# Kernel optimization log

Hardware: AMD Instinct MI355X
Metric: run time of the kernel (lower is better)

## Reference

```python
import jax, jax.numpy as jnp
import numpy as np
from jax import lax

BETA = 0.5        # Sinkhron beta
N_ITER = 20       # got_iteration
THRESH = 0.1      # P > 0.1 threshold
NL_I = 5          # apply_non_linearity(..., 'elu', i=5)
EPS = 1e-9


def setup_inputs() -> dict:
    key = jax.random.key(0)
    k1, k2 = jax.random.split(key)
    B, N, D = 128, 512, 128
    h = jax.random.normal(k1, (B, N, D), dtype=jnp.float32)
    W0 = jnp.ones((D,), dtype=jnp.float32)
    W1 = jnp.ones((D,), dtype=jnp.float32)
    lengths = jax.random.randint(k2, (B,), 0, N, dtype=jnp.int32)
    return {"h": h, "W0": W0, "W1": W1, "lengths": lengths}


def _forward(h, W0, W1, lengths):
    B, N, D = h.shape
    lengths = jnp.maximum(lengths, 1)
    mask = (jnp.arange(N)[None, :] < lengths[:, None])          # [B, N] bool
    mf = mask.astype(h.dtype)
    mask2 = mf[:, :, None] * mf[:, None, :]                      # [B, N, N]

    # internal_forward: Diag layers with relu between (mlp_act='relu')
    h = h * W0
    h = jax.nn.relu(h)
    h = h * W1

    # cost_matrix_batch_torch: cosine similarity, add identity diag, mask
    hn = h / (jnp.linalg.norm(h, axis=-1, keepdims=True) + 1e-12)
    sim = jnp.einsum('bnd,bmd->bnm', hn, hn)                     # [B, N, N]
    sim = sim + jnp.eye(N, dtype=h.dtype)                        # add_eye_diag
    sim = sim * mask2
    cost = (1.0 - sim) * mask2

    # Sinkhorn with uniform marginals on valid nodes, fixed iterations
    n = lengths.astype(h.dtype)
    mu = mf / n[:, None]                                         # [B, N]
    K = jnp.exp(-cost / BETA) * mask2                            # [B, N, N]

    def body(carry, _):
        u, v = carry
        u = mu / (jnp.einsum('bnm,bm->bn', K, v) + EPS) * mf
        v = mu / (jnp.einsum('bnm,bn->bm', K, u) + EPS) * mf
        return (u, v), None

    (u, v), _ = lax.scan(body, (mf, mf), None, length=N_ITER)
    P = u[:, :, None] * K * v[:, None, :]                        # transport plan

    # P.detach(); scale by number of nodes per graph; threshold
    P = lax.stop_gradient(P)
    P = n[:, None, None] * P
    A = (P > THRESH).astype(h.dtype)
    similarity = A * sim
    # apply_non_linearity 'elu': elu(x*i - i) + 1
    out = jax.nn.elu(similarity * NL_I - NL_I) + 1.0
    return out


def reference(h, W0, W1, lengths):
    return _forward(h, W0, W1, lengths)
```

## Files before the change

kernel.cpp:

```cpp
#include <hip/hip_runtime.h>

#define BB 128
#define NN 512
#define DD 128
#define SLOT_STRIDE 544

__global__ __launch_bounds__(256) void hn_kernel(const float* __restrict__ h,
                                                 const float* __restrict__ W0,
                                                 const float* __restrict__ W1,
                                                 float* __restrict__ hn) {
    int wave = (int)((blockIdx.x * blockDim.x + threadIdx.x) >> 6);
    int lane = threadIdx.x & 63;
    const float2* h2 = (const float2*)(h + (size_t)wave * DD);
    float2 w0 = ((const float2*)W0)[lane];
    float2 w1 = ((const float2*)W1)[lane];
    float2 x = h2[lane];
    float p0 = fmaxf(x.x * w0.x, 0.0f) * w1.x;
    float p1 = fmaxf(x.y * w0.y, 0.0f) * w1.y;
    float ss = p0 * p0 + p1 * p1;
#pragma unroll
    for (int m = 32; m; m >>= 1) ss += __shfl_xor(ss, m);
    float inv = 1.0f / (sqrtf(ss) + 1e-12f);
    float2 o;
    o.x = p0 * inv;
    o.y = p1 * inv;
    ((float2*)(hn + (size_t)wave * DD))[lane] = o;
}

#define KC 32
__global__ __launch_bounds__(256) void sim_kernel(const float* __restrict__ hn,
                                                  const int* __restrict__ lengths,
                                                  float* __restrict__ K) {
    __shared__ float As[KC][132];
    __shared__ float Bs[KC][132];
    __shared__ int pre[BB + 1];
    int tid = threadIdx.x;
    if (tid == 0) {
        int acc = 0;
        for (int b = 0; b < BB; b++) {
            pre[b] = acc;
            int len = max(lengths[b], 1);
            int nt = (len + 127) >> 7;
            acc += nt * nt;
        }
        pre[BB] = acc;
    }
    __syncthreads();
    int total = pre[BB];

    int lr = tid >> 3;
    int lk = (tid & 7) << 2;
    int tx = tid & 15, ty = tid >> 4;

    for (int t = blockIdx.x; t < total; t += gridDim.x) {
        int lo = 0, hi = BB;
        while (lo + 1 < hi) {
            int mid = (lo + hi) >> 1;
            if (pre[mid] <= t) lo = mid; else hi = mid;
        }
        int b = lo;
        int local = t - pre[b];
        int len = max(lengths[b], 1);
        int nt = (len + 127) >> 7;
        int ti = local / nt;
        int tj = local - ti * nt;
        int r0 = ti << 7, c0 = tj << 7;
        const float* base = hn + (size_t)b * NN * DD;
        float acc[8][8] = {};

        for (int kc = 0; kc < DD; kc += KC) {
#pragma unroll
            for (int rr = 0; rr < 128; rr += 32) {
                float4 a = *(const float4*)(base + (size_t)(r0 + lr + rr) * DD + kc + lk);
                As[lk + 0][lr + rr] = a.x; As[lk + 1][lr + rr] = a.y;
                As[lk + 2][lr + rr] = a.z; As[lk + 3][lr + rr] = a.w;
                float4 bb = *(const float4*)(base + (size_t)(c0 + lr + rr) * DD + kc + lk);
                Bs[lk + 0][lr + rr] = bb.x; Bs[lk + 1][lr + rr] = bb.y;
                Bs[lk + 2][lr + rr] = bb.z; Bs[lk + 3][lr + rr] = bb.w;
            }
            __syncthreads();
#pragma unroll
            for (int kk = 0; kk < KC; kk++) {
                float4 a0 = *(const float4*)&As[kk][ty * 8];
                float4 a1 = *(const float4*)&As[kk][ty * 8 + 4];
                float4 b0 = *(const float4*)&Bs[kk][tx * 4];
                float4 b1 = *(const float4*)&Bs[kk][64 + tx * 4];
                float ar[8] = {a0.x, a0.y, a0.z, a0.w, a1.x, a1.y, a1.z, a1.w};
                float bc[8] = {b0.x, b0.y, b0.z, b0.w, b1.x, b1.y, b1.z, b1.w};
#pragma unroll
                for (int r = 0; r < 8; r++)
#pragma unroll
                    for (int c = 0; c < 8; c++)
                        acc[r][c] = fmaf(ar[r], bc[c], acc[r][c]);
            }
            __syncthreads();
        }
        float* out = K + (size_t)b * NN * NN;
#pragma unroll
        for (int r = 0; r < 8; r++) {
            int i = r0 + ty * 8 + r;
            if (i >= len) continue;
#pragma unroll
            for (int cg = 0; cg < 2; cg++) {
                int j0 = c0 + cg * 64 + tx * 4;
                if (j0 >= len) continue;
                float vv[4];
#pragma unroll
                for (int c = 0; c < 4; c++) {
                    float s = acc[r][cg * 4 + c] + ((i == j0 + c) ? 1.0f : 0.0f);
                    vv[c] = expf(2.0f * s - 2.0f);
                }
                float4 o;
                o.x = vv[0]; o.y = vv[1]; o.z = vv[2]; o.w = vv[3];
                *(float4*)(out + (size_t)i * NN + j0) = o;
            }
        }
    }
}

__device__ __forceinline__ float dot8(float4 A, float4 B, float4 x0, float4 x1) {
    float d = fmaf(A.x, x0.x, fmaf(A.y, x0.y, fmaf(A.z, x0.z, A.w * x0.w)));
    return fmaf(B.x, x1.x, fmaf(B.y, x1.y, fmaf(B.z, x1.z, fmaf(B.w, x1.w, d))));
}

__global__ __launch_bounds__(512, 4) void coop_sink(const float* __restrict__ K,
                                                    float* __restrict__ u_buf,
                                                    float* __restrict__ v_buf,
                                                    const int* __restrict__ lengths,
                                                    float* __restrict__ slots) {
    __shared__ float xb[NN];
    __shared__ float pv[8 * NN];
    __shared__ int Sh[16], Pre[16];

    int g = blockIdx.x;
    int x = g & 7;
    int j = g >> 3;
    int tid = threadIdx.x;

    if (tid == 0) {
        int need[16]; int ssum = 0;
        for (int m = 0; m < 16; m++) {
            int L = max(lengths[x + 8 * m], 1);
            need[m] = (L + 63) >> 6;
            ssum += need[m];
        }
        while (ssum > 64) {
            int best = 0, bv = need[0];
            for (int m = 1; m < 16; m++)
                if (need[m] > bv) { bv = need[m]; best = m; }
            need[best]--; ssum--;
        }
        int acc = 0;
        for (int m = 0; m < 16; m++) { Pre[m] = acc; Sh[m] = need[m]; acc += need[m]; }
    }
    __syncthreads();

    int m = -1;
    for (int mm = 0; mm < 16; mm++)
        if (j >= Pre[mm] && j < Pre[mm] + Sh[mm]) { m = mm; break; }
    if (m < 0) return;
    int b = x + 8 * m;
    int q = j - Pre[m];
    int S = Sh[m];
    int jbase = Pre[m];

    int len = max(lengths[b], 1);
    int len4 = (len + 3) & ~3;
    int rpq = (len + S - 1) / S;
    int r_lo = q * rpq;
    int nrows = min(len - r_lo, rpq);
    if (nrows < 0) nrows = 0;
    float inv_n = 1.0f / (float)len;

    int w = tid >> 6, l = tid & 63;
    int c0 = 4 * l, c1 = 256 + 4 * l;
    bool a0 = c0 < len4, a1 = c1 < len4;
    const float* Kb = K + (size_t)b * NN * NN;

    xb[tid] = (tid < len) ? 1.0f : 0.0f;

    float4 kA0 = {0,0,0,0}, kA1 = {0,0,0,0}, kA2 = {0,0,0,0}, kA3 = {0,0,0,0};
    float4 kA4 = {0,0,0,0}, kA5 = {0,0,0,0}, kA6 = {0,0,0,0}, kA7 = {0,0,0,0};
    float4 kB0 = {0,0,0,0}, kB1 = {0,0,0,0}, kB2 = {0,0,0,0}, kB3 = {0,0,0,0};
    float4 kB4 = {0,0,0,0}, kB5 = {0,0,0,0}, kB6 = {0,0,0,0}, kB7 = {0,0,0,0};
#define FILL_ROW(o)                                                          \
    {                                                                        \
        int i_ = w + 8 * o;                                                  \
        if (i_ < nrows) {                                                    \
            const float* g0_ = Kb + (size_t)(r_lo + i_) * NN;                \
            if (a0) kA##o = *(const float4*)(g0_ + c0);                      \
            if (a1) kB##o = *(const float4*)(g0_ + c1);                      \
        }                                                                    \
    }
    FILL_ROW(0) FILL_ROW(1) FILL_ROW(2) FILL_ROW(3)
    FILL_ROW(4) FILL_ROW(5) FILL_ROW(6) FILL_ROW(7)
#undef FILL_ROW

    __syncthreads();

    for (int t = 0; t < 20; t++) {
        float4 xv0 = *(const float4*)(xb + c0);
        float4 xv1 = *(const float4*)(xb + c1);
        float4 pa = {0, 0, 0, 0}, pb = {0, 0, 0, 0};

        float d0 = dot8(kA0, kB0, xv0, xv1);
        float d1 = dot8(kA1, kB1, xv0, xv1);
        float d2 = dot8(kA2, kB2, xv0, xv1);
        float d3 = dot8(kA3, kB3, xv0, xv1);
        float d4 = dot8(kA4, kB4, xv0, xv1);
        float d5 = dot8(kA5, kB5, xv0, xv1);
        float d6 = dot8(kA6, kB6, xv0, xv1);
        float d7 = dot8(kA7, kB7, xv0, xv1);
#pragma unroll
        for (int mm = 32; mm; mm >>= 1) {
            d0 += __shfl_xor(d0, mm); d1 += __shfl_xor(d1, mm);
            d2 += __shfl_xor(d2, mm); d3 += __shfl_xor(d3, mm);
            d4 += __shfl_xor(d4, mm); d5 += __shfl_xor(d5, mm);
            d6 += __shfl_xor(d6, mm); d7 += __shfl_xor(d7, mm);
        }
        float u0 = inv_n / (d0 + 1e-9f), u1 = inv_n / (d1 + 1e-9f);
        float u2 = inv_n / (d2 + 1e-9f), u3 = inv_n / (d3 + 1e-9f);
        float u4 = inv_n / (d4 + 1e-9f), u5 = inv_n / (d5 + 1e-9f);
        float u6 = inv_n / (d6 + 1e-9f), u7 = inv_n / (d7 + 1e-9f);
#define ACC_ROW(o, uo)                                                       \
    pa.x = fmaf(kA##o.x, uo, pa.x); pa.y = fmaf(kA##o.y, uo, pa.y);          \
    pa.z = fmaf(kA##o.z, uo, pa.z); pa.w = fmaf(kA##o.w, uo, pa.w);          \
    pb.x = fmaf(kB##o.x, uo, pb.x); pb.y = fmaf(kB##o.y, uo, pb.y);          \
    pb.z = fmaf(kB##o.z, uo, pb.z); pb.w = fmaf(kB##o.w, uo, pb.w);
        ACC_ROW(0, u0) ACC_ROW(1, u1) ACC_ROW(2, u2) ACC_ROW(3, u3)
        ACC_ROW(4, u4) ACC_ROW(5, u5) ACC_ROW(6, u6) ACC_ROW(7, u7)
#undef ACC_ROW
        if (t == 19 && l == 0) {
            float* ub = u_buf + (size_t)b * NN + r_lo + w;
            if (w + 0 < nrows) ub[0] = u0;
            if (w + 8 < nrows) ub[8] = u1;
            if (w + 16 < nrows) ub[16] = u2;
            if (w + 24 < nrows) ub[24] = u3;
            if (w + 32 < nrows) ub[32] = u4;
            if (w + 40 < nrows) ub[40] = u5;
            if (w + 48 < nrows) ub[48] = u6;
            if (w + 56 < nrows) ub[56] = u7;
        }

        for (int i = 64 + w; i < nrows; i += 8) {
            const float* g0 = Kb + (size_t)(r_lo + i) * NN;
            float4 A = {0, 0, 0, 0}, B = {0, 0, 0, 0};
            if (a0) A = *(const float4*)(g0 + c0);
            if (a1) B = *(const float4*)(g0 + c1);
            float d = dot8(A, B, xv0, xv1);
#pragma unroll
            for (int mm = 32; mm; mm >>= 1) d += __shfl_xor(d, mm);
            float uu = inv_n / (d + 1e-9f);
            pa.x = fmaf(A.x, uu, pa.x); pa.y = fmaf(A.y, uu, pa.y);
            pa.z = fmaf(A.z, uu, pa.z); pa.w = fmaf(A.w, uu, pa.w);
            pb.x = fmaf(B.x, uu, pb.x); pb.y = fmaf(B.y, uu, pb.y);
            pb.z = fmaf(B.z, uu, pb.z); pb.w = fmaf(B.w, uu, pb.w);
            if (t == 19 && l == 0) u_buf[(size_t)b * NN + r_lo + i] = uu;
        }

        *(float4*)(pv + w * NN + c0) = pa;
        *(float4*)(pv + w * NN + c1) = pb;
        __syncthreads();
        float* slotp = slots + ((size_t)(t & 1) * 512 + g) * SLOT_STRIDE;
        int c = tid;
        float s0 = pv[c] + pv[NN + c] + pv[2 * NN + c] + pv[3 * NN + c] +
                   pv[4 * NN + c] + pv[5 * NN + c] + pv[6 * NN + c] + pv[7 * NN + c];
        __hip_atomic_store(slotp + c, s0, __ATOMIC_RELAXED, __HIP_MEMORY_SCOPE_AGENT);
        asm volatile("s_waitcnt vmcnt(0)" ::: "memory");
        __syncthreads();
        if (tid == 0)
            __hip_atomic_store((int*)(slotp + 512), t + 1, __ATOMIC_RELAXED,
                               __HIP_MEMORY_SCOPE_AGENT);
        if (tid < S && tid != q) {
            const int* tagp = (const int*)(slots +
                ((size_t)(t & 1) * 512 + (size_t)(x + 8 * (jbase + tid))) * SLOT_STRIDE + 512);
            while (__hip_atomic_load(tagp, __ATOMIC_RELAXED, __HIP_MEMORY_SCOPE_AGENT) != t + 1)
                __builtin_amdgcn_s_sleep(1);
        }
        __syncthreads();

        const float* sbase = slots + ((size_t)(t & 1) * 512) * SLOT_STRIDE;
        float t0 = s0;
        for (int s = 1; s < S; s++) {
            int k = q + s; if (k >= S) k -= S;
            t0 += __hip_atomic_load(sbase + (size_t)(x + 8 * (jbase + k)) * SLOT_STRIDE + c,
                                    __ATOMIC_RELAXED, __HIP_MEMORY_SCOPE_AGENT);
        }
        float v0 = (c < len) ? (inv_n / (t0 + 1e-9f)) : 0.0f;
        if (t < 19) {
            xb[c] = v0;
        } else if (c >= r_lo && c < r_lo + nrows) {
            v_buf[(size_t)b * NN + c] = v0;
        }
        __syncthreads();
    }
}

__global__ __launch_bounds__(256) void epi_kernel(float* __restrict__ io,
                                                  const float* __restrict__ u,
                                                  const float* __restrict__ v,
                                                  const int* __restrict__ lengths) {
    const float E5 = 0.006737946999085467f;
    size_t idx = (size_t)blockIdx.x * 256 + threadIdx.x;
    int b = (int)(idx >> 16);
    int r = (int)(idx >> 7) & (NN - 1);
    int c4 = ((int)idx & 127) << 2;
    int len = max(lengths[b], 1);
    float4 o;
    if (r >= len || c4 >= len) {
        o.x = E5; o.y = E5; o.z = E5; o.w = E5;
        ((float4*)io)[idx] = o;
        return;
    }
    float4 k = ((float4*)io)[idx];
    float ui = u[(size_t)b * NN + r];
    float4 vv = *(const float4*)(v + (size_t)b * NN + c4);
    float t = (float)len * ui;
    float kv[4] = {k.x, k.y, k.z, k.w};
    float vj[4] = {vv.x, vv.y, vv.z, vv.w};
    float ov[4];
#pragma unroll
    for (int c = 0; c < 4; c++) {
        float Kc = kv[c];
        float P = t * Kc * vj[c];
        bool valid = (c4 + c) < len;
        if (valid && P > 0.1f) {
            float x = 2.5f * logf(Kc);
            ov[c] = (x > 0.0f) ? (x + 1.0f) : expf(x);
        } else {
            ov[c] = E5;
        }
    }
    o.x = ov[0]; o.y = ov[1]; o.z = ov[2]; o.w = ov[3];
    ((float4*)io)[idx] = o;
}

extern "C" void kernel_launch(void* const* d_in, const int* in_sizes, int n_in,
                              void* d_out, int out_size, void* d_ws, size_t ws_size,
                              hipStream_t stream) {
    const float* h = (const float*)d_in[0];
    const float* W0 = (const float*)d_in[1];
    const float* W1 = (const float*)d_in[2];
    const int* lengths = (const int*)d_in[3];
    float* K = (float*)d_out;

    char* ws = (char*)d_ws;
    float* hn = (float*)ws;
    size_t off = (size_t)BB * NN * DD * 4;
    float* u = (float*)(ws + off);     off += (size_t)BB * NN * 4;
    float* v = (float*)(ws + off);     off += (size_t)BB * NN * 4;
    float* slots = (float*)(ws + off); off += (size_t)2 * 512 * SLOT_STRIDE * 4;

    hn_kernel<<<BB * NN / 4, 256, 0, stream>>>(h, W0, W1, hn);
    sim_kernel<<<1024, 256, 0, stream>>>(hn, lengths, K);

    coop_sink<<<512, 512, 0, stream>>>(K, u, v, lengths, slots);

    epi_kernel<<<(unsigned)((size_t)BB * NN * NN / 4 / 256), 256, 0, stream>>>(K, u, v, lengths);
}
```

Measured before the change: 382.1 us.

## Balance Sinkhorn row partitions across all batches with 80-row register tiles

```diff
diff --git a/kernel.cpp b/kernel.cpp
--- a/kernel.cpp
+++ b/kernel.cpp
@@ -130,39 +130,37 @@
                                                     float* __restrict__ slots) {
     __shared__ float xb[NN];
     __shared__ float pv[8 * NN];
-    __shared__ int Sh[16], Pre[16];
+    __shared__ int Sh[BB], Pre[BB];
 
     int g = blockIdx.x;
-    int x = g & 7;
-    int j = g >> 3;
     int tid = threadIdx.x;
 
     if (tid == 0) {
-        int need[16]; int ssum = 0;
-        for (int m = 0; m < 16; m++) {
-            int L = max(lengths[x + 8 * m], 1);
-            need[m] = (L + 63) >> 6;
+        int need[BB]; int ssum = 0;
+        for (int m = 0; m < BB; m++) {
+            int L = max(lengths[m], 1);
+            need[m] = (L + 79) / 80;
             ssum += need[m];
         }
-        while (ssum > 64) {
+        while (ssum > 512) {
             int best = 0, bv = need[0];
-            for (int m = 1; m < 16; m++)
+            for (int m = 1; m < BB; m++)
                 if (need[m] > bv) { bv = need[m]; best = m; }
             need[best]--; ssum--;
         }
         int acc = 0;
-        for (int m = 0; m < 16; m++) { Pre[m] = acc; Sh[m] = need[m]; acc += need[m]; }
+        for (int m = 0; m < BB; m++) { Pre[m] = acc; Sh[m] = need[m]; acc += need[m]; }
     }
     __syncthreads();
 
     int m = -1;
-    for (int mm = 0; mm < 16; mm++)
-        if (j >= Pre[mm] && j < Pre[mm] + Sh[mm]) { m = mm; break; }
+    for (int mm = 0; mm < BB; mm++)
+        if (g >= Pre[mm] && g < Pre[mm] + Sh[mm]) { m = mm; break; }
     if (m < 0) return;
-    int b = x + 8 * m;
-    int q = j - Pre[m];
+    int b = m;
+    int jbase = Pre[m];
+    int q = g - jbase;
     int S = Sh[m];
-    int jbase = Pre[m];
 
     int len = max(lengths[b], 1);
     int len4 = (len + 3) & ~3;
@@ -181,8 +179,10 @@
 
     float4 kA0 = {0,0,0,0}, kA1 = {0,0,0,0}, kA2 = {0,0,0,0}, kA3 = {0,0,0,0};
     float4 kA4 = {0,0,0,0}, kA5 = {0,0,0,0}, kA6 = {0,0,0,0}, kA7 = {0,0,0,0};
+    float4 kA8 = {0,0,0,0}, kA9 = {0,0,0,0};
     float4 kB0 = {0,0,0,0}, kB1 = {0,0,0,0}, kB2 = {0,0,0,0}, kB3 = {0,0,0,0};
     float4 kB4 = {0,0,0,0}, kB5 = {0,0,0,0}, kB6 = {0,0,0,0}, kB7 = {0,0,0,0};
+    float4 kB8 = {0,0,0,0}, kB9 = {0,0,0,0};
 #define FILL_ROW(o)                                                          \
     {                                                                        \
         int i_ = w + 8 * o;                                                  \
@@ -192,8 +192,8 @@
             if (a1) kB##o = *(const float4*)(g0_ + c1);                      \
         }                                                                    \
     }
-    FILL_ROW(0) FILL_ROW(1) FILL_ROW(2) FILL_ROW(3)
-    FILL_ROW(4) FILL_ROW(5) FILL_ROW(6) FILL_ROW(7)
+    FILL_ROW(0) FILL_ROW(1) FILL_ROW(2) FILL_ROW(3) FILL_ROW(4)
+    FILL_ROW(5) FILL_ROW(6) FILL_ROW(7) FILL_ROW(8) FILL_ROW(9)
 #undef FILL_ROW
 
     __syncthreads();
@@ -211,17 +211,21 @@
         float d5 = dot8(kA5, kB5, xv0, xv1);
         float d6 = dot8(kA6, kB6, xv0, xv1);
         float d7 = dot8(kA7, kB7, xv0, xv1);
+        float d8 = dot8(kA8, kB8, xv0, xv1);
+        float d9 = dot8(kA9, kB9, xv0, xv1);
 #pragma unroll
         for (int mm = 32; mm; mm >>= 1) {
             d0 += __shfl_xor(d0, mm); d1 += __shfl_xor(d1, mm);
             d2 += __shfl_xor(d2, mm); d3 += __shfl_xor(d3, mm);
             d4 += __shfl_xor(d4, mm); d5 += __shfl_xor(d5, mm);
             d6 += __shfl_xor(d6, mm); d7 += __shfl_xor(d7, mm);
+            d8 += __shfl_xor(d8, mm); d9 += __shfl_xor(d9, mm);
         }
         float u0 = inv_n / (d0 + 1e-9f), u1 = inv_n / (d1 + 1e-9f);
         float u2 = inv_n / (d2 + 1e-9f), u3 = inv_n / (d3 + 1e-9f);
         float u4 = inv_n / (d4 + 1e-9f), u5 = inv_n / (d5 + 1e-9f);
         float u6 = inv_n / (d6 + 1e-9f), u7 = inv_n / (d7 + 1e-9f);
+        float u8 = inv_n / (d8 + 1e-9f), u9 = inv_n / (d9 + 1e-9f);
 #define ACC_ROW(o, uo)                                                       \
     pa.x = fmaf(kA##o.x, uo, pa.x); pa.y = fmaf(kA##o.y, uo, pa.y);          \
     pa.z = fmaf(kA##o.z, uo, pa.z); pa.w = fmaf(kA##o.w, uo, pa.w);          \
@@ -229,6 +233,7 @@
     pb.z = fmaf(kB##o.z, uo, pb.z); pb.w = fmaf(kB##o.w, uo, pb.w);
         ACC_ROW(0, u0) ACC_ROW(1, u1) ACC_ROW(2, u2) ACC_ROW(3, u3)
         ACC_ROW(4, u4) ACC_ROW(5, u5) ACC_ROW(6, u6) ACC_ROW(7, u7)
+        ACC_ROW(8, u8) ACC_ROW(9, u9)
 #undef ACC_ROW
         if (t == 19 && l == 0) {
             float* ub = u_buf + (size_t)b * NN + r_lo + w;
@@ -240,9 +245,11 @@
             if (w + 40 < nrows) ub[40] = u5;
             if (w + 48 < nrows) ub[48] = u6;
             if (w + 56 < nrows) ub[56] = u7;
-        }
-
-        for (int i = 64 + w; i < nrows; i += 8) {
+            if (w + 64 < nrows) ub[64] = u8;
+            if (w + 72 < nrows) ub[72] = u9;
+        }
+
+        for (int i = 80 + w; i < nrows; i += 8) {
             const float* g0 = Kb + (size_t)(r_lo + i) * NN;
             float4 A = {0, 0, 0, 0}, B = {0, 0, 0, 0};
             if (a0) A = *(const float4*)(g0 + c0);
@@ -273,7 +280,7 @@
                                __HIP_MEMORY_SCOPE_AGENT);
         if (tid < S && tid != q) {
             const int* tagp = (const int*)(slots +
-                ((size_t)(t & 1) * 512 + (size_t)(x + 8 * (jbase + tid))) * SLOT_STRIDE + 512);
+                ((size_t)(t & 1) * 512 + (size_t)(jbase + tid)) * SLOT_STRIDE + 512);
             while (__hip_atomic_load(tagp, __ATOMIC_RELAXED, __HIP_MEMORY_SCOPE_AGENT) != t + 1)
                 __builtin_amdgcn_s_sleep(1);
         }
@@ -283,7 +290,7 @@
         float t0 = s0;
         for (int s = 1; s < S; s++) {
             int k = q + s; if (k >= S) k -= S;
-            t0 += __hip_atomic_load(sbase + (size_t)(x + 8 * (jbase + k)) * SLOT_STRIDE + c,
+            t0 += __hip_atomic_load(sbase + (size_t)(jbase + k) * SLOT_STRIDE + c,
                                     __ATOMIC_RELAXED, __HIP_MEMORY_SCOPE_AGENT);
         }
         float v0 = (c < len) ? (inv_n / (t0 + 1e-9f)) : 0.0f;
```

Result: slower. 393.9 us (+3.1%).
